# Optimization experiments

Measured on AMD Instinct MI355X. Metric: run time of the kernel, lower is better.

The kernel has to match this reference:

```python
import jax, jax.numpy as jnp
import numpy as np

B, N, W, D = 32, 576, 32, 256  # batch, patches, max concepts per sample, embed dim


def _l2norm(x, eps=1e-12):
    # matches torch F.normalize: x / max(||x||, eps)
    n = jnp.linalg.norm(x, axis=-1, keepdims=True)
    return x / jnp.maximum(n, eps)


def setup_inputs() -> dict:
    key = jax.random.key(0)
    k1, k2, k3 = jax.random.split(key, 3)
    return {
        "image_token_features": jax.random.normal(k1, (B, N, D), dtype=jnp.float32),
        "concept_text_features": jax.random.normal(k2, (B, W, D), dtype=jnp.float32),
        "concept_lengths": jax.random.randint(k3, (B,), 1, W + 1, dtype=jnp.int32),
        "logit_scale": jnp.array([2.0], dtype=jnp.float32),   # log-scale, clamp(-10,10).exp()
        "logit_bias": jnp.array([-1.0], dtype=jnp.float32),
    }


def reference(image_token_features, concept_text_features, logit_scale, logit_bias, concept_lengths):
    img = _l2norm(image_token_features)          # (B, N, D)
    con = _l2norm(concept_text_features)         # (B, W, D)
    # A[m, c, n, w] = cos(patch_n of image m, concept_w of sample c)
    A = jnp.einsum('mnd,cwd->mcnw', img, con)    # (B, B, N, W) -- dominant intermediate
    max_per_concept = A.max(axis=2)              # max over patches -> (B, B, W)
    # masked mean over valid concepts (ragged lengths)
    mask = (jnp.arange(W)[None, :] < concept_lengths[:, None]).astype(img.dtype)  # (B, W)
    lens = concept_lengths.astype(img.dtype)     # all >= 1 by construction
    sim = jnp.sum(max_per_concept * mask[None, :, :], axis=-1) / lens[None, :]    # (B, B)
    t = jnp.exp(jnp.clip(logit_scale, -10.0, 10.0))[0]
    logits = jnp.clip(t * sim + logit_bias[0], -50.0, 50.0)
    z = 2.0 * jnp.eye(sim.shape[0], dtype=sim.dtype) - 1.0  # +1 diag, -1 off-diag
    loss = -jnp.mean(jax.nn.log_sigmoid(z * logits))
    return loss
```

## Files before the change

kernel.cpp:

```cpp
#include <hip/hip_runtime.h>
#include <hip/hip_bf16.h>
#include <math.h>

#define BB 32
#define NP 576
#define WW 32
#define DD 256

typedef __bf16 bf16x8 __attribute__((ext_vector_type(8)));
typedef float f32x4 __attribute__((ext_vector_type(4)));

__device__ __forceinline__ unsigned short f2bf(float f) {
  unsigned int u = __float_as_uint(f);
  u += 0x7FFFu + ((u >> 16) & 1u);
  return (unsigned short)(u >> 16);
}

__global__ __launch_bounds__(256) void norm_cast_kernel(
    const float* __restrict__ img, const float* __restrict__ con,
    unsigned short* __restrict__ img_bf, unsigned short* __restrict__ con_bf) {
  int row = blockIdx.x * 4 + (threadIdx.x >> 6);
  int lane = threadIdx.x & 63;
  const int n_img = BB * NP;
  const float* src;
  unsigned short* dst;
  if (row < n_img) {
    src = img + (size_t)row * DD;
    dst = img_bf + (size_t)row * DD;
  } else {
    int r2 = row - n_img;
    src = con + (size_t)r2 * DD;
    dst = con_bf + (size_t)r2 * DD;
  }
  float4 v = ((const float4*)src)[lane];
  float ss = v.x * v.x + v.y * v.y + v.z * v.z + v.w * v.w;
  #pragma unroll
  for (int off = 1; off < 64; off <<= 1) ss += __shfl_xor(ss, off);
  float inv = 1.0f / fmaxf(sqrtf(ss), 1e-12f);
  ushort4 o;
  o.x = f2bf(v.x * inv);
  o.y = f2bf(v.y * inv);
  o.z = f2bf(v.z * inv);
  o.w = f2bf(v.w * inv);
  ((ushort4*)dst)[lane] = o;
}

__global__ __launch_bounds__(256, 3) void gemm_max_kernel(
    const unsigned short* __restrict__ img_bf,
    const unsigned short* __restrict__ con_bf,
    float* __restrict__ P) {
  int bx = blockIdx.x;
  int bw = bx & 7;
  int bm = bx >> 3;
  int m = bm / 5;
  int t = bm - m * 5;
  int p0 = m * NP + t * 128;
  int w0 = bw * 128;

  __shared__ __align__(16) unsigned char lds[33 * 1024];
  unsigned char* ldsA = lds;
  unsigned char* ldsB = lds + 16384;
  float* sm = (float*)(lds + 32768);

  int tid = threadIdx.x;
  int wid = tid >> 6;
  int lane = tid & 63;
  int q = lane >> 4;
  int r = lane & 15;
  int wp = wid >> 1;
  int wc = wid & 1;

  f32x4 acc[4][4];
  #pragma unroll
  for (int i = 0; i < 4; ++i)
    #pragma unroll
    for (int j = 0; j < 4; ++j) acc[i][j] = (f32x4){0.f, 0.f, 0.f, 0.f};

  for (int kb = 0; kb < 4; ++kb) {
    __syncthreads();
    uint4 va[4], vb[4];
    #pragma unroll
    for (int j = 0; j < 4; ++j) {
      int g = j * 256 + tid;
      int row = g >> 3;
      int s = g & 7;
      va[j] = *(const uint4*)(img_bf + (size_t)(p0 + row) * DD + kb * 64 + s * 8);
      vb[j] = *(const uint4*)(con_bf + (size_t)(w0 + row) * DD + kb * 64 + s * 8);
    }
    #pragma unroll
    for (int j = 0; j < 4; ++j) {
      int g = j * 256 + tid;
      int row = g >> 3;
      int s = g & 7;
      int sw = ((s ^ (row & 7)) << 4);
      *(uint4*)(ldsA + row * 128 + sw) = va[j];
      *(uint4*)(ldsB + row * 128 + sw) = vb[j];
    }
    __syncthreads();
    #pragma unroll
    for (int kk = 0; kk < 2; ++kk) {
      bf16x8 af[4], bfr[4];
      int sw = ((((kk << 2) | q) ^ (r & 7)) << 4);
      #pragma unroll
      for (int pi = 0; pi < 4; ++pi) {
        int arow = wp * 64 + pi * 16 + r;
        af[pi] = *(const bf16x8*)(ldsA + arow * 128 + sw);
      }
      #pragma unroll
      for (int wj = 0; wj < 4; ++wj) {
        int brow = wc * 64 + wj * 16 + r;
        bfr[wj] = *(const bf16x8*)(ldsB + brow * 128 + sw);
      }
      #pragma unroll
      for (int pi = 0; pi < 4; ++pi)
        #pragma unroll
        for (int wj = 0; wj < 4; ++wj)
          acc[pi][wj] =
              __builtin_amdgcn_mfma_f32_16x16x32_bf16(af[pi], bfr[wj], acc[pi][wj], 0, 0, 0);
    }
  }

  float mxw[4];
  #pragma unroll
  for (int wj = 0; wj < 4; ++wj) {
    float v = -1e30f;
    #pragma unroll
    for (int pi = 0; pi < 4; ++pi) {
      v = fmaxf(v, fmaxf(fmaxf(acc[pi][wj][0], acc[pi][wj][1]),
                         fmaxf(acc[pi][wj][2], acc[pi][wj][3])));
    }
    v = fmaxf(v, __shfl_xor(v, 16));
    v = fmaxf(v, __shfl_xor(v, 32));
    mxw[wj] = v;
  }
  __syncthreads();
  if (lane < 16) {
    #pragma unroll
    for (int wj = 0; wj < 4; ++wj)
      sm[wp * 128 + wc * 64 + wj * 16 + lane] = mxw[wj];
  }
  __syncthreads();
  if (tid < 128) {
    float v = sm[tid];
    if (t != 4) v = fmaxf(v, sm[128 + tid]);
    P[(size_t)bm * 1024 + w0 + tid] = v;
  }
}

__global__ __launch_bounds__(256) void reduce_kernel(
    const float* __restrict__ P, const int* __restrict__ lengths,
    float* __restrict__ sims) {
  int pair = blockIdx.x * 4 + (threadIdx.x >> 6);
  int lane = threadIdx.x & 63;
  int m = pair >> 5;
  int c = pair & 31;
  int w = lane & 31;
  const float* base = P + (size_t)(m * 5) * 1024 + c * 32 + w;
  float v = base[0];
  v = fmaxf(v, base[1024]);
  v = fmaxf(v, base[2048]);
  v = fmaxf(v, base[3072]);
  v = fmaxf(v, base[4096]);
  int len = lengths[c];
  float contrib = (w < len) ? v : 0.0f;
  #pragma unroll
  for (int off = 1; off < 32; off <<= 1) contrib += __shfl_xor(contrib, off);
  if (lane == 0) sims[pair] = contrib / (float)len;
}

__global__ __launch_bounds__(256) void loss_kernel(
    const float* __restrict__ sims, const float* __restrict__ lscale,
    const float* __restrict__ lbias, float* __restrict__ out) {
  float tt = expf(fminf(fmaxf(lscale[0], -10.0f), 10.0f));
  float bias = lbias[0];
  int tid = threadIdx.x;
  float acc = 0.0f;
  for (int p = tid; p < BB * BB; p += 256) {
    int mm = p >> 5;
    int cc = p & 31;
    float lg = fminf(fmaxf(tt * sims[p] + bias, -50.0f), 50.0f);
    float x = (mm == cc) ? lg : -lg;
    float ls = (x >= 0.0f) ? -log1pf(expf(-x)) : (x - log1pf(expf(x)));
    acc += ls;
  }
  #pragma unroll
  for (int off = 1; off < 64; off <<= 1) acc += __shfl_xor(acc, off);
  __shared__ float s[4];
  if ((tid & 63) == 0) s[tid >> 6] = acc;
  __syncthreads();
  if (tid == 0) out[0] = -(s[0] + s[1] + s[2] + s[3]) / (float)(BB * BB);
}

extern "C" void kernel_launch(void* const* d_in, const int* in_sizes, int n_in,
                              void* d_out, int out_size, void* d_ws, size_t ws_size,
                              hipStream_t stream) {
  const float* img = (const float*)d_in[0];
  const float* con = (const float*)d_in[1];
  const int* lens = (const int*)d_in[2];
  const float* lsc = (const float*)d_in[3];
  const float* lbi = (const float*)d_in[4];

  unsigned short* img_bf = (unsigned short*)d_ws;
  unsigned short* con_bf = img_bf + (size_t)BB * NP * DD;
  float* P = (float*)(con_bf + (size_t)BB * WW * DD);
  float* sims = P + (size_t)160 * 1024;

  norm_cast_kernel<<<(BB * NP + BB * WW) / 4, 256, 0, stream>>>(img, con, img_bf, con_bf);
  gemm_max_kernel<<<160 * 8, 256, 0, stream>>>(img_bf, con_bf, P);
  reduce_kernel<<<256, 256, 0, stream>>>(P, lens, sims);
  loss_kernel<<<1, 256, 0, stream>>>(sims, lsc, lbi, (float*)d_out);
}
```

Measured before the change: 96.12 us.

## Use direct global-to-LDS loads and retile patch rows contiguously across images

Tile loads now use global_load_lds, so data goes straight from global memory into LDS. The XOR swizzle is applied by permuting the global source address rather than the LDS destination, which removes the register staging and the separate LDS store loop. The patch dimension is treated as one flattened B*N range and split into 144 full 128-row tiles. This replaces the 160 tiles in which every fifth was only half used. The epilogue maps each 64-row half to its image slot, so P keeps the same five-slot-per-image layout the reduce kernel expects, at the cost of some integer index arithmetic.

Result: no change. 95.10 us (-1.1%).

```diff
diff --git a/kernel.cpp b/kernel.cpp
--- a/kernel.cpp
+++ b/kernel.cpp
@@ -52,9 +52,7 @@
   int bx = blockIdx.x;
   int bw = bx & 7;
   int bm = bx >> 3;
-  int m = bm / 5;
-  int t = bm - m * 5;
-  int p0 = m * NP + t * 128;
+  int R0 = bm * 128;
   int w0 = bw * 128;
 
   __shared__ __align__(16) unsigned char lds[33 * 1024];
@@ -78,23 +76,21 @@
 
   for (int kb = 0; kb < 4; ++kb) {
     __syncthreads();
-    uint4 va[4], vb[4];
     #pragma unroll
     for (int j = 0; j < 4; ++j) {
-      int g = j * 256 + tid;
+      int g = j * 256 + wid * 64 + lane;
       int row = g >> 3;
-      int s = g & 7;
-      va[j] = *(const uint4*)(img_bf + (size_t)(p0 + row) * DD + kb * 64 + s * 8);
-      vb[j] = *(const uint4*)(con_bf + (size_t)(w0 + row) * DD + kb * 64 + s * 8);
-    }
-    #pragma unroll
-    for (int j = 0; j < 4; ++j) {
-      int g = j * 256 + tid;
-      int row = g >> 3;
-      int s = g & 7;
-      int sw = ((s ^ (row & 7)) << 4);
-      *(uint4*)(ldsA + row * 128 + sw) = va[j];
-      *(uint4*)(ldsB + row * 128 + sw) = vb[j];
+      int sl = (g & 7) ^ (row & 7);
+      const unsigned short* ga = img_bf + (size_t)(R0 + row) * DD + kb * 64 + sl * 8;
+      const unsigned short* gb = con_bf + (size_t)(w0 + row) * DD + kb * 64 + sl * 8;
+      unsigned char* la = ldsA + (j * 256 + wid * 64) * 16;
+      unsigned char* lb = ldsB + (j * 256 + wid * 64) * 16;
+      __builtin_amdgcn_global_load_lds(
+          (const __attribute__((address_space(1))) unsigned int*)ga,
+          (__attribute__((address_space(3))) unsigned int*)la, 16, 0, 0);
+      __builtin_amdgcn_global_load_lds(
+          (const __attribute__((address_space(1))) unsigned int*)gb,
+          (__attribute__((address_space(3))) unsigned int*)lb, 16, 0, 0);
     }
     __syncthreads();
     #pragma unroll
@@ -141,9 +137,17 @@
   }
   __syncthreads();
   if (tid < 128) {
-    float v = sm[tid];
-    if (t != 4) v = fmaxf(v, sm[128 + tid]);
-    P[(size_t)bm * 1024 + w0 + tid] = v;
+    int i0 = (2 * bm) / 9;
+    int slot = bm - (9 * i0) / 2;
+    bool crossing = ((2 * bm) % 9) == 8;
+    float vlo = sm[tid];
+    float vhi = sm[128 + tid];
+    if (crossing) {
+      P[(size_t)(i0 * 5 + slot) * 1024 + w0 + tid] = vlo;
+      P[(size_t)((i0 + 1) * 5) * 1024 + w0 + tid] = vhi;
+    } else {
+      P[(size_t)(i0 * 5 + slot) * 1024 + w0 + tid] = fmaxf(vlo, vhi);
+    }
   }
 }
 
@@ -206,7 +210,7 @@
   float* sims = P + (size_t)160 * 1024;
 
   norm_cast_kernel<<<(BB * NP + BB * WW) / 4, 256, 0, stream>>>(img, con, img_bf, con_bf);
-  gemm_max_kernel<<<160 * 8, 256, 0, stream>>>(img_bf, con_bf, P);
+  gemm_max_kernel<<<144 * 8, 256, 0, stream>>>(img_bf, con_bf, P);
   reduce_kernel<<<256, 256, 0, stream>>>(P, lens, sims);
   loss_kernel<<<1, 256, 0, stream>>>(sims, lsc, lbi, (float*)d_out);
 }
```
